# Performance work log

Hardware: AMD Instinct MI355X
Metric: run time of the kernel (lower is better)

The kernel has to match this reference:

```python
import jax, jax.numpy as jnp
import numpy as np

MARGIN = 0.35


def setup_inputs() -> dict:
    key = jax.random.key(0)
    k1, k2 = jax.random.split(key)
    N, D = 8192, 512
    inp = jax.random.normal(k1, (N, D), dtype=jnp.float32)
    label = jax.random.randint(k2, (N,), 0, D, dtype=jnp.int64)
    return {"input": inp, "label": label}


def reference(input, label):
    N = input.shape[0]
    # Faithful to the torch code: squared-norm terms use L2-normalized input,
    # but the -2*x@x.T cross term uses the UNnormalized input (original quirk).
    x_norm = input / jnp.linalg.norm(input, axis=1, keepdims=True)
    sq = jnp.sum(x_norm * x_norm, axis=1, keepdims=True)  # [N,1]
    dist = sq + sq.T - 2.0 * (input @ input.T)            # [N,N]
    mask = label[:, None] == label[None, :]               # same-label mask
    neg_inf = jnp.array(-jnp.inf, dist.dtype)
    pos_inf = jnp.array(jnp.inf, dist.dtype)
    # hardest positive (max over same-label), hardest negative (min over diff-label)
    positive_part = jnp.max(jnp.where(mask, dist, neg_inf), axis=1)
    negative_part = jnp.min(jnp.where(mask, pos_inf, dist), axis=1)
    triplet = jnp.mean(jnp.maximum(positive_part - negative_part + MARGIN, 0.0))
    # cross entropy: input are logits, label class indices
    logz = jax.nn.logsumexp(input, axis=1)
    true_logit = jnp.take_along_axis(input, label[:, None].astype(jnp.int32), axis=1)[:, 0]
    ce = jnp.mean(logz - true_logit)
    return triplet + ce
```

## Files before the change

kernel.cpp:

```cpp
#include <hip/hip_runtime.h>
#include <hip/hip_bf16.h>
#include <stdint.h>

#define N_ROWS 8192
#define DIM 512
#define NLAB 512
#define MARGIN_F 0.35f
#define NBLK 64
#define NPURE 1953
#define NDIAG 127
#define NTILE (NPURE + NDIAG)
#define ROWSTAT_BLOCKS (N_ROWS / 4)

typedef __attribute__((ext_vector_type(4))) float floatx4;
typedef __attribute__((ext_vector_type(8))) int intx8;

__device__ __forceinline__ unsigned enc_f(float f) {
    unsigned u = __float_as_uint(f);
    return (u & 0x80000000u) ? ~u : (u | 0x80000000u);
}
__device__ __forceinline__ float dec_f(unsigned e) {
    unsigned u = (e & 0x80000000u) ? (e ^ 0x80000000u) : ~e;
    return __uint_as_float(u);
}

__device__ __forceinline__ void load_lds16(const void* g, void* l) {
    __builtin_amdgcn_global_load_lds((__attribute__((address_space(1))) void*)(void*)g,
                                     (__attribute__((address_space(3))) void*)l, 16, 0, 0);
}

__global__ __launch_bounds__(512) void histscan_kernel(const int* __restrict__ label,
                                                       int* __restrict__ offsetArr,
                                                       int* __restrict__ cnt,
                                                       float* __restrict__ out) {
    __shared__ int h[NLAB];
    __shared__ int sc[NLAB];
    int t = threadIdx.x;
    h[t] = 0;
    __syncthreads();
    for (int i = t; i < N_ROWS; i += 512) atomicAdd(&h[label[i]], 1);
    __syncthreads();
    int v = h[t];
    sc[t] = v;
    __syncthreads();
    for (int d = 1; d < NLAB; d <<= 1) {
        int add = (t >= d) ? sc[t - d] : 0;
        __syncthreads();
        sc[t] += add;
        __syncthreads();
    }
    offsetArr[t] = sc[t] - v;
    cnt[t] = 0;
    if (t == 0) out[0] = 0.f;
}

__global__ __launch_bounds__(256) void rowstats_kernel(const float* __restrict__ x,
                                                       const int* __restrict__ label,
                                                       const int* __restrict__ offsetArr,
                                                       int* __restrict__ cnt,
                                                       unsigned char* __restrict__ a8,
                                                       int* __restrict__ sortedLabel,
                                                       float* __restrict__ cePartial,
                                                       unsigned* __restrict__ minEnc,
                                                       unsigned* __restrict__ maxEnc) {
    int gid = blockIdx.x * 256 + threadIdx.x;
    if (gid < N_ROWS) { minEnc[gid] = 0xFFFFFFFFu; maxEnc[gid] = 0u; }

    int w = threadIdx.x >> 6;
    int row = blockIdx.x * 4 + w;
    int l = threadIdx.x & 63;
    const float* xr = x + (size_t)row * DIM;
    float4 v0 = ((const float4*)xr)[2 * l];
    float4 v1 = ((const float4*)xr)[2 * l + 1];
    float vals[8] = {v0.x, v0.y, v0.z, v0.w, v1.x, v1.y, v1.z, v1.w};

    float mx = vals[0];
#pragma unroll
    for (int i = 1; i < 8; i++) mx = fmaxf(mx, vals[i]);
#pragma unroll
    for (int s = 1; s < 64; s <<= 1) mx = fmaxf(mx, __shfl_xor(mx, s, 64));

    float se = 0.f;
#pragma unroll
    for (int i = 0; i < 8; i++) se += expf(vals[i] - mx);
#pragma unroll
    for (int s = 1; s < 64; s <<= 1) se += __shfl_xor(se, s, 64);

    int pos = 0;
    if (l == 0) {
        int lab = label[row];
        pos = offsetArr[lab] + atomicAdd(&cnt[lab], 1);
        sortedLabel[pos] = lab;
    }
    pos = __shfl(pos, 0, 64);

    int w0 = __builtin_amdgcn_cvt_pk_fp8_f32(vals[0], vals[1], 0, false);
    w0 = __builtin_amdgcn_cvt_pk_fp8_f32(vals[2], vals[3], w0, true);
    int w1 = __builtin_amdgcn_cvt_pk_fp8_f32(vals[4], vals[5], 0, false);
    w1 = __builtin_amdgcn_cvt_pk_fp8_f32(vals[6], vals[7], w1, true);
    ((uint2*)(a8 + (size_t)pos * DIM))[l] = make_uint2((unsigned)w0, (unsigned)w1);

    __shared__ float wsum[4];
    if (l == 0) {
        float tl = xr[label[row]];
        wsum[w] = mx + logf(se) - tl;
    }
    __syncthreads();
    if (threadIdx.x == 0)
        cePartial[blockIdx.x] = wsum[0] + wsum[1] + wsum[2] + wsum[3];
}

__global__ __launch_bounds__(256, 2) void gemm_kernel(const unsigned char* __restrict__ A,
                                                      const int* __restrict__ sortedLabel,
                                                      unsigned* __restrict__ minEnc,
                                                      unsigned* __restrict__ maxEnc) {
    __shared__ unsigned char As[2][128 * 128];
    __shared__ unsigned char Bs[2][128 * 128];
    __shared__ float redA[128][2], redB[128][2];

    int b = blockIdx.x;
    bool diag = (b < NDIAG);
    int bi, bj;
    if (diag) {
        bi = (b < 64) ? b : (b - 63);
        bj = (b < 64) ? b : (b - 64);
    } else {
        int p = b - NDIAG;
        int ci = (int)((sqrtf(8.0f * (float)p + 1.0f) - 1.0f) * 0.5f);
        while ((ci + 1) * (ci + 2) / 2 <= p) ci++;
        while (ci * (ci + 1) / 2 > p) ci--;
        bj = p - ci * (ci + 1) / 2;
        bi = ci + 2;
    }
    int ibase = bi * 128, jbase = bj * 128;

    int t = threadIdx.x;
    int w = t >> 6, l = t & 63;
    int wm = w >> 1, wn = w & 1;
    int q = l >> 4, lm = l & 15;

    floatx4 acc[4][4];
#pragma unroll
    for (int a = 0; a < 4; a++)
#pragma unroll
        for (int c = 0; c < 4; c++) acc[a][c] = (floatx4)0.f;

    int s_r = t >> 3;
    int s_c = ((t & 7) ^ (s_r & 7));

#define STAGE(KK, BUF)                                                                     \
    {                                                                                      \
        int k0_ = (KK) * 128;                                                              \
        _Pragma("unroll") for (int i2 = 0; i2 < 4; i2++) {                                 \
            int r_ = i2 * 32 + s_r;                                                        \
            int slot_ = (i2 * 256 + t) * 16;                                               \
            load_lds16(A + (size_t)(ibase + r_) * DIM + k0_ + s_c * 16, As[BUF] + slot_);  \
            load_lds16(A + (size_t)(jbase + r_) * DIM + k0_ + s_c * 16, Bs[BUF] + slot_);  \
        }                                                                                  \
    }

    STAGE(0, 0);
    __syncthreads();

#pragma unroll
    for (int kk = 0; kk < 4; kk++) {
        int cur = kk & 1;
        if (kk < 3) STAGE(kk + 1, cur ^ 1);

        intx8 bfv[4];
#pragma unroll
        for (int tn = 0; tn < 4; tn++) {
            int R = wn * 64 + tn * 16 + lm;
            const int4* rowp = (const int4*)(Bs[cur] + R * 128);
            int4 lo = rowp[(2 * q) ^ (R & 7)];
            int4 hi = rowp[(2 * q + 1) ^ (R & 7)];
            intx8 v;
            v[0] = lo.x; v[1] = lo.y; v[2] = lo.z; v[3] = lo.w;
            v[4] = hi.x; v[5] = hi.y; v[6] = hi.z; v[7] = hi.w;
            bfv[tn] = v;
        }
#pragma unroll
        for (int tm = 0; tm < 4; tm++) {
            int R = wm * 64 + tm * 16 + lm;
            const int4* rowp = (const int4*)(As[cur] + R * 128);
            int4 lo = rowp[(2 * q) ^ (R & 7)];
            int4 hi = rowp[(2 * q + 1) ^ (R & 7)];
            intx8 af;
            af[0] = lo.x; af[1] = lo.y; af[2] = lo.z; af[3] = lo.w;
            af[4] = hi.x; af[5] = hi.y; af[6] = hi.z; af[7] = hi.w;
#pragma unroll
            for (int tn = 0; tn < 4; tn++)
                acc[tm][tn] = __builtin_amdgcn_mfma_scale_f32_16x16x128_f8f6f4(
                    af, bfv[tn], acc[tm][tn], 0, 0,
                    0, 0x7F7F7F7F,
                    0, 0x7F7F7F7F);
        }
        __syncthreads();
    }
#undef STAGE

    const float INF = __builtin_inff();

    if (!diag) {
        float mxJ[4];
#pragma unroll
        for (int tn = 0; tn < 4; tn++) mxJ[tn] = -INF;
#pragma unroll
        for (int tm = 0; tm < 4; tm++) {
#pragma unroll
            for (int r = 0; r < 4; r++) {
                int row_l = wm * 64 + tm * 16 + q * 4 + r;
                float mxI = -INF;
#pragma unroll
                for (int tn = 0; tn < 4; tn++) {
                    float v = acc[tm][tn][r];
                    mxI = fmaxf(mxI, v);
                    mxJ[tn] = fmaxf(mxJ[tn], v);
                }
#pragma unroll
                for (int s = 1; s < 16; s <<= 1)
                    mxI = fmaxf(mxI, __shfl_xor(mxI, s, 64));
                if (lm == 0) redA[row_l][wn] = mxI;
            }
        }
#pragma unroll
        for (int tn = 0; tn < 4; tn++) {
#pragma unroll
            for (int s = 16; s < 64; s <<= 1)
                mxJ[tn] = fmaxf(mxJ[tn], __shfl_xor(mxJ[tn], s, 64));
            if (q == 0) redB[wn * 64 + tn * 16 + lm][wm] = mxJ[tn];
        }
        __syncthreads();
        if (t < 128) {
            atomicMax(&maxEnc[ibase + t], enc_f(fmaxf(redA[t][0], redA[t][1])));
            atomicMax(&maxEnc[jbase + t], enc_f(fmaxf(redB[t][0], redB[t][1])));
        }
    } else {
        int* labi = (int*)&As[0][0];
        int* labj = labi + 128;
        float (*redImn)[2] = (float (*)[2])(labj + 128);
        float (*redJmn)[2] = redImn + 128;
        if (t < 128) labi[t] = sortedLabel[ibase + t];
        else labj[t - 128] = sortedLabel[jbase + t - 128];
        __syncthreads();

        int jlab[4];
#pragma unroll
        for (int tn = 0; tn < 4; tn++) jlab[tn] = labj[wn * 64 + tn * 16 + lm];

        float mnJ[4], mxJ[4];
#pragma unroll
        for (int tn = 0; tn < 4; tn++) { mnJ[tn] = INF; mxJ[tn] = -INF; }

#pragma unroll
        for (int tm = 0; tm < 4; tm++) {
#pragma unroll
            for (int r = 0; r < 4; r++) {
                int row_l = wm * 64 + tm * 16 + q * 4 + r;
                int il = labi[row_l];
                float mnI = INF, mxI = -INF;
#pragma unroll
                for (int tn = 0; tn < 4; tn++) {
                    float v = acc[tm][tn][r];
                    bool same = (jlab[tn] == il);
                    float vs = same ? v : INF;
                    float vd = same ? -INF : v;
                    mnI = fminf(mnI, vs);
                    mxI = fmaxf(mxI, vd);
                    mnJ[tn] = fminf(mnJ[tn], vs);
                    mxJ[tn] = fmaxf(mxJ[tn], vd);
                }
#pragma unroll
                for (int s = 1; s < 16; s <<= 1) {
                    mnI = fminf(mnI, __shfl_xor(mnI, s, 64));
                    mxI = fmaxf(mxI, __shfl_xor(mxI, s, 64));
                }
                if (lm == 0) { redImn[row_l][wn] = mnI; redA[row_l][wn] = mxI; }
            }
        }
#pragma unroll
        for (int tn = 0; tn < 4; tn++) {
#pragma unroll
            for (int s = 16; s < 64; s <<= 1) {
                mnJ[tn] = fminf(mnJ[tn], __shfl_xor(mnJ[tn], s, 64));
                mxJ[tn] = fmaxf(mxJ[tn], __shfl_xor(mxJ[tn], s, 64));
            }
            if (q == 0) {
                int col_l = wn * 64 + tn * 16 + lm;
                redJmn[col_l][wm] = mnJ[tn];
                redB[col_l][wm] = mxJ[tn];
            }
        }
        __syncthreads();
        if (t < 128) {
            atomicMin(&minEnc[ibase + t], enc_f(fminf(redImn[t][0], redImn[t][1])));
            atomicMax(&maxEnc[ibase + t], enc_f(fmaxf(redA[t][0], redA[t][1])));
            atomicMin(&minEnc[jbase + t], enc_f(fminf(redJmn[t][0], redJmn[t][1])));
            atomicMax(&maxEnc[jbase + t], enc_f(fmaxf(redB[t][0], redB[t][1])));
        }
    }
}

__global__ __launch_bounds__(256) void finalize_kernel(const unsigned* __restrict__ minEnc,
                                                       const unsigned* __restrict__ maxEnc,
                                                       const float* __restrict__ cePartial,
                                                       float* __restrict__ out) {
    int gid = blockIdx.x * 256 + threadIdx.x;
    float mn = dec_f(minEnc[gid]);
    float mxv = dec_f(maxEnc[gid]);
    float s = fmaxf(2.0f * (mxv - mn) + MARGIN_F, 0.f);
    if (gid < ROWSTAT_BLOCKS) s += cePartial[gid];
#pragma unroll
    for (int sh = 1; sh < 64; sh <<= 1) s += __shfl_xor(s, sh, 64);
    __shared__ float red[4];
    int w = threadIdx.x >> 6, l = threadIdx.x & 63;
    if (l == 0) red[w] = s;
    __syncthreads();
    if (threadIdx.x == 0)
        atomicAdd(out, (red[0] + red[1] + red[2] + red[3]) * (1.0f / (float)N_ROWS));
}

extern "C" void kernel_launch(void* const* d_in, const int* in_sizes, int n_in,
                              void* d_out, int out_size, void* d_ws, size_t ws_size,
                              hipStream_t stream) {
    const float* x = (const float*)d_in[0];
    const int* label = (const int*)d_in[1];
    float* out = (float*)d_out;

    char* ws = (char*)d_ws;
    unsigned char* a8 = (unsigned char*)ws;
    char* p = ws + (size_t)N_ROWS * DIM;
    unsigned* minEnc = (unsigned*)p;            p += N_ROWS * 4;
    unsigned* maxEnc = (unsigned*)p;            p += N_ROWS * 4;
    float* cePartial = (float*)p;               p += ROWSTAT_BLOCKS * 4;
    int* offsetArr = (int*)p;                   p += NLAB * 4;
    int* cnt = (int*)p;                         p += NLAB * 4;
    int* sortedLabel = (int*)p;                 p += N_ROWS * 4;

    histscan_kernel<<<1, 512, 0, stream>>>(label, offsetArr, cnt, out);
    rowstats_kernel<<<ROWSTAT_BLOCKS, 256, 0, stream>>>(x, label, offsetArr, cnt, a8,
                                                        sortedLabel, cePartial, minEnc, maxEnc);
    gemm_kernel<<<NTILE, 256, 0, stream>>>(a8, sortedLabel, minEnc, maxEnc);
    finalize_kernel<<<32, 256, 0, stream>>>(minEnc, maxEnc, cePartial, out);
}
```

Before: 119.5 us.

## Load GEMM fp8 fragments directly from global memory, drop LDS staging

Removes the double-buffered LDS staging of A/B tiles through global_load_lds and has each wave read its MFMA operand fragments straight from global memory into registers. Label and reduction scratch arrays become dedicated small shared buffers instead of aliasing the tile buffers, and occupancy hint rises to 3 blocks per CU. This cuts LDS traffic and block-wide barriers but relies on L2/L1 to serve the data reuse that LDS provided, and direct loads may be less coalesced and duplicated across waves.

```diff
diff --git a/kernel.cpp b/kernel.cpp
--- a/kernel.cpp
+++ b/kernel.cpp
@@ -22,11 +22,6 @@
 __device__ __forceinline__ float dec_f(unsigned e) {
     unsigned u = (e & 0x80000000u) ? (e ^ 0x80000000u) : ~e;
     return __uint_as_float(u);
-}
-
-__device__ __forceinline__ void load_lds16(const void* g, void* l) {
-    __builtin_amdgcn_global_load_lds((__attribute__((address_space(1))) void*)(void*)g,
-                                     (__attribute__((address_space(3))) void*)l, 16, 0, 0);
 }
 
 __global__ __launch_bounds__(512) void histscan_kernel(const int* __restrict__ label,
@@ -110,13 +105,13 @@
         cePartial[blockIdx.x] = wsum[0] + wsum[1] + wsum[2] + wsum[3];
 }
 
-__global__ __launch_bounds__(256, 2) void gemm_kernel(const unsigned char* __restrict__ A,
+__global__ __launch_bounds__(256, 3) void gemm_kernel(const unsigned char* __restrict__ A,
                                                       const int* __restrict__ sortedLabel,
                                                       unsigned* __restrict__ minEnc,
                                                       unsigned* __restrict__ maxEnc) {
-    __shared__ unsigned char As[2][128 * 128];
-    __shared__ unsigned char Bs[2][128 * 128];
     __shared__ float redA[128][2], redB[128][2];
+    __shared__ float redImn[128][2], redJmn[128][2];
+    __shared__ int labi[128], labj[128];
 
     int b = blockIdx.x;
     bool diag = (b < NDIAG);
@@ -139,41 +134,27 @@
     int wm = w >> 1, wn = w & 1;
     int q = l >> 4, lm = l & 15;
 
+    if (diag) {
+        if (t < 128) labi[t] = sortedLabel[ibase + t];
+        else labj[t - 128] = sortedLabel[jbase + t - 128];
+    }
+
     floatx4 acc[4][4];
 #pragma unroll
     for (int a = 0; a < 4; a++)
 #pragma unroll
         for (int c = 0; c < 4; c++) acc[a][c] = (floatx4)0.f;
 
-    int s_r = t >> 3;
-    int s_c = ((t & 7) ^ (s_r & 7));
-
-#define STAGE(KK, BUF)                                                                     \
-    {                                                                                      \
-        int k0_ = (KK) * 128;                                                              \
-        _Pragma("unroll") for (int i2 = 0; i2 < 4; i2++) {                                 \
-            int r_ = i2 * 32 + s_r;                                                        \
-            int slot_ = (i2 * 256 + t) * 16;                                               \
-            load_lds16(A + (size_t)(ibase + r_) * DIM + k0_ + s_c * 16, As[BUF] + slot_);  \
-            load_lds16(A + (size_t)(jbase + r_) * DIM + k0_ + s_c * 16, Bs[BUF] + slot_);  \
-        }                                                                                  \
-    }
-
-    STAGE(0, 0);
-    __syncthreads();
+    const int4* pA = (const int4*)(A + (size_t)(ibase + wm * 64 + lm) * DIM + q * 32);
+    const int4* pB = (const int4*)(A + (size_t)(jbase + wn * 64 + lm) * DIM + q * 32);
 
 #pragma unroll
     for (int kk = 0; kk < 4; kk++) {
-        int cur = kk & 1;
-        if (kk < 3) STAGE(kk + 1, cur ^ 1);
-
         intx8 bfv[4];
 #pragma unroll
         for (int tn = 0; tn < 4; tn++) {
-            int R = wn * 64 + tn * 16 + lm;
-            const int4* rowp = (const int4*)(Bs[cur] + R * 128);
-            int4 lo = rowp[(2 * q) ^ (R & 7)];
-            int4 hi = rowp[(2 * q + 1) ^ (R & 7)];
+            int4 lo = pB[tn * 512 + kk * 8];
+            int4 hi = pB[tn * 512 + kk * 8 + 1];
             intx8 v;
             v[0] = lo.x; v[1] = lo.y; v[2] = lo.z; v[3] = lo.w;
             v[4] = hi.x; v[5] = hi.y; v[6] = hi.z; v[7] = hi.w;
@@ -181,10 +162,8 @@
         }
 #pragma unroll
         for (int tm = 0; tm < 4; tm++) {
-            int R = wm * 64 + tm * 16 + lm;
-            const int4* rowp = (const int4*)(As[cur] + R * 128);
-            int4 lo = rowp[(2 * q) ^ (R & 7)];
-            int4 hi = rowp[(2 * q + 1) ^ (R & 7)];
+            int4 lo = pA[tm * 512 + kk * 8];
+            int4 hi = pA[tm * 512 + kk * 8 + 1];
             intx8 af;
             af[0] = lo.x; af[1] = lo.y; af[2] = lo.z; af[3] = lo.w;
             af[4] = hi.x; af[5] = hi.y; af[6] = hi.z; af[7] = hi.w;
@@ -195,9 +174,7 @@
                     0, 0x7F7F7F7F,
                     0, 0x7F7F7F7F);
         }
-        __syncthreads();
-    }
-#undef STAGE
+    }
 
     const float INF = __builtin_inff();
 
@@ -236,12 +213,6 @@
             atomicMax(&maxEnc[jbase + t], enc_f(fmaxf(redB[t][0], redB[t][1])));
         }
     } else {
-        int* labi = (int*)&As[0][0];
-        int* labj = labi + 128;
-        float (*redImn)[2] = (float (*)[2])(labj + 128);
-        float (*redJmn)[2] = redImn + 128;
-        if (t < 128) labi[t] = sortedLabel[ibase + t];
-        else labj[t - 128] = sortedLabel[jbase + t - 128];
         __syncthreads();
 
         int jlab[4];
```

New measurement: 151.5 us. +26.8%, slower.

## Single-buffer GEMM LDS, raise occupancy to three blocks, and remap block order across XCDs

Applied to the files above, without the earlier changes.

Replaces the double-buffered LDS staging with a single buffer that is loaded and synchronized each k-step. This halves shared memory, and launch bounds now request three blocks per CU. Block indices are also permuted so diagonal and off-diagonal tiles are spread across XCDs. The trade is losing intra-block overlap of global loads with MFMA work in exchange for more concurrent blocks and better balance.

```diff
diff --git a/kernel.cpp b/kernel.cpp
--- a/kernel.cpp
+++ b/kernel.cpp
@@ -110,15 +110,16 @@
         cePartial[blockIdx.x] = wsum[0] + wsum[1] + wsum[2] + wsum[3];
 }
 
-__global__ __launch_bounds__(256, 2) void gemm_kernel(const unsigned char* __restrict__ A,
+__global__ __launch_bounds__(256, 3) void gemm_kernel(const unsigned char* __restrict__ A,
                                                       const int* __restrict__ sortedLabel,
                                                       unsigned* __restrict__ minEnc,
                                                       unsigned* __restrict__ maxEnc) {
-    __shared__ unsigned char As[2][128 * 128];
-    __shared__ unsigned char Bs[2][128 * 128];
+    __shared__ unsigned char As[128 * 128];
+    __shared__ unsigned char Bs[128 * 128];
     __shared__ float redA[128][2], redB[128][2];
 
     int b = blockIdx.x;
+    b = (b & 7) * (NTILE / 8) + (b >> 3);
     bool diag = (b < NDIAG);
     int bi, bj;
     if (diag) {
@@ -148,30 +149,22 @@
     int s_r = t >> 3;
     int s_c = ((t & 7) ^ (s_r & 7));
 
-#define STAGE(KK, BUF)                                                                     \
-    {                                                                                      \
-        int k0_ = (KK) * 128;                                                              \
-        _Pragma("unroll") for (int i2 = 0; i2 < 4; i2++) {                                 \
-            int r_ = i2 * 32 + s_r;                                                        \
-            int slot_ = (i2 * 256 + t) * 16;                                               \
-            load_lds16(A + (size_t)(ibase + r_) * DIM + k0_ + s_c * 16, As[BUF] + slot_);  \
-            load_lds16(A + (size_t)(jbase + r_) * DIM + k0_ + s_c * 16, Bs[BUF] + slot_);  \
-        }                                                                                  \
-    }
-
-    STAGE(0, 0);
-    __syncthreads();
-
-#pragma unroll
     for (int kk = 0; kk < 4; kk++) {
-        int cur = kk & 1;
-        if (kk < 3) STAGE(kk + 1, cur ^ 1);
+        int k0 = kk * 128;
+#pragma unroll
+        for (int i2 = 0; i2 < 4; i2++) {
+            int r = i2 * 32 + s_r;
+            int slot = (i2 * 256 + t) * 16;
+            load_lds16(A + (size_t)(ibase + r) * DIM + k0 + s_c * 16, As + slot);
+            load_lds16(A + (size_t)(jbase + r) * DIM + k0 + s_c * 16, Bs + slot);
+        }
+        __syncthreads();
 
         intx8 bfv[4];
 #pragma unroll
         for (int tn = 0; tn < 4; tn++) {
             int R = wn * 64 + tn * 16 + lm;
-            const int4* rowp = (const int4*)(Bs[cur] + R * 128);
+            const int4* rowp = (const int4*)(Bs + R * 128);
             int4 lo = rowp[(2 * q) ^ (R & 7)];
             int4 hi = rowp[(2 * q + 1) ^ (R & 7)];
             intx8 v;
@@ -182,7 +175,7 @@
 #pragma unroll
         for (int tm = 0; tm < 4; tm++) {
             int R = wm * 64 + tm * 16 + lm;
-            const int4* rowp = (const int4*)(As[cur] + R * 128);
+            const int4* rowp = (const int4*)(As + R * 128);
             int4 lo = rowp[(2 * q) ^ (R & 7)];
             int4 hi = rowp[(2 * q + 1) ^ (R & 7)];
             intx8 af;
@@ -197,7 +190,6 @@
         }
         __syncthreads();
     }
-#undef STAGE
 
     const float INF = __builtin_inff();
 
@@ -236,7 +228,7 @@
             atomicMax(&maxEnc[jbase + t], enc_f(fmaxf(redB[t][0], redB[t][1])));
         }
     } else {
-        int* labi = (int*)&As[0][0];
+        int* labi = (int*)As;
         int* labj = labi + 128;
         float (*redImn)[2] = (float (*)[2])(labj + 128);
         float (*redJmn)[2] = redImn + 128;
```

Result: faster. 112.5 us (-5.9%).
